# Kernel optimization log

Measured on AMD Instinct MI355X. Metric: run time of the kernel, lower is better.

## Reference

```python
import jax, jax.numpy as jnp
import numpy as np

B = 8
N_PER = 8192   # xyz points per batch
M_PER = 2048   # query points per batch
C_FEAT = 32
RADIUS = 0.2
K = 32         # sample_nums
USE_XYZ = True


def setup_inputs() -> dict:
    key = jax.random.key(0)
    k1, k2, k3 = jax.random.split(key, 3)
    xyz = jax.random.uniform(k1, (B * N_PER, 3), dtype=jnp.float32)
    new_xyz = jax.random.uniform(k2, (B * M_PER, 3), dtype=jnp.float32)
    features = jax.random.normal(k3, (B * N_PER, C_FEAT), dtype=jnp.float32)
    xyz_batch_cnt = jnp.full((B,), N_PER, dtype=jnp.int32)
    new_xyz_batch_cnt = jnp.full((B,), M_PER, dtype=jnp.int32)
    return {
        "xyz": xyz,
        "xyz_batch_cnt": xyz_batch_cnt,
        "new_xyz": new_xyz,
        "new_xyz_batch_cnt": new_xyz_batch_cnt,
        "features": features,
    }


def _ball_query(xyz_b, new_b, radius, k):
    # xyz_b: (B, N, 3), new_b: (B, M, 3)
    n = xyz_b.shape[1]
    # squared pairwise distances (B, M, N)
    d2 = jnp.sum((new_b[:, :, None, :] - xyz_b[:, None, :, :]) ** 2, axis=-1)
    mask = d2 < (radius * radius)
    # first-k in-radius indices (CUDA ball_query keeps neighbors in point order)
    scores = jnp.where(mask, jnp.arange(n, dtype=jnp.int32), jnp.int32(n))
    idx_sorted = jnp.sort(scores, axis=-1)[..., :k]          # (B, M, k)
    cnt = jnp.sum(mask, axis=-1)                              # (B, M)
    empty = cnt == 0                                          # (B, M)
    first = idx_sorted[..., :1]                               # duplicate first hit
    slot = jnp.arange(k, dtype=jnp.int32)
    idx = jnp.where(slot[None, None, :] < cnt[..., None], idx_sorted, first)
    idx = jnp.where(empty[..., None], jnp.int32(0), idx)      # empty balls -> 0
    return idx, empty


def reference(xyz, xyz_batch_cnt, new_xyz, new_xyz_batch_cnt, features):
    b = xyz_batch_cnt.shape[0]
    xyz_b = xyz.reshape(b, -1, 3)          # (B, N, 3)
    new_b = new_xyz.reshape(b, -1, 3)      # (B, M, 3)
    feat_b = features.reshape(b, xyz_b.shape[1], -1)  # (B, N, C)

    idx, empty = _ball_query(xyz_b, new_b, RADIUS, K)  # (B, M, K), (B, M)

    gather = jax.vmap(lambda pts, i: pts[i])           # per-batch gather
    grouped_xyz = gather(xyz_b, idx) - new_b[:, :, None, :]   # (B, M, K, 3)
    grouped_xyz = jnp.where(empty[..., None, None], 0.0, grouped_xyz)

    grouped_feat = gather(feat_b, idx)                        # (B, M, K, C)
    grouped_feat = jnp.where(empty[..., None, None], 0.0, grouped_feat)

    if USE_XYZ:
        new_features = jnp.concatenate([grouped_xyz, grouped_feat], axis=-1)
    else:
        new_features = grouped_feat
    # (B, M, K, 3+C) -> (B*M, 3+C, K) to match torch (Mtot, C', nsample)
    m_tot = b * new_b.shape[1]
    new_features = jnp.transpose(new_features, (0, 1, 3, 2)).reshape(
        m_tot, -1, K)
    idx_flat = idx.reshape(m_tot, K)
    return new_features, idx_flat
```

## Files before the change

kernel.cpp:

```cpp
#include <hip/hip_runtime.h>

#define BATCHES   8
#define N_PER     8192
#define M_PER     2048
#define C_FEAT    32
#define KNN       32
#define R2        0.04f
#define M_TOT     (BATCHES * M_PER)
#define FEAT_OUT  (3 + C_FEAT)
#define OUT_FEAT_SZ ((size_t)M_TOT * FEAT_OUT * KNN)

__global__ __launch_bounds__(256) void sqag_fused_kernel(
    const float* __restrict__ xyz,
    const float* __restrict__ new_xyz,
    const float* __restrict__ features,
    float* __restrict__ out)
{
    __shared__ int sidx[4][KNN];

    const int wave = threadIdx.x >> 6;
    const int lane = threadIdx.x & 63;

    const int bswz   = blockIdx.x & 7;
    const int within = blockIdx.x >> 3;
    const int q = __builtin_amdgcn_readfirstlane(
        (bswz * (M_PER / 4) + within) * 4 + wave);
    const int b    = q >> 11;
    const int base = b * N_PER;

    const float px = new_xyz[q * 3 + 0];
    const float py = new_xyz[q * 3 + 1];
    const float pz = new_xyz[q * 3 + 2];

    int cnt = 0;
    int first = 0;

    const float4* pb = (const float4*)(xyz + (size_t)base * 3) + lane * 3;
    float4 c0 = pb[0], c1 = pb[1], c2 = pb[2];

    for (int cb = 0;;) {
        const bool more = (cb + 256) < N_PER;
        float4 n0, n1, n2;
        if (more) {
            const float4* pn = pb + 192;
            n0 = pn[0]; n1 = pn[1]; n2 = pn[2];
        }

        const float X[4] = { c0.x, c0.w, c1.z, c2.y };
        const float Y[4] = { c0.y, c1.x, c1.w, c2.z };
        const float Z[4] = { c0.z, c1.y, c2.x, c2.w };

        unsigned long long m[4];
        bool in[4];
        #pragma unroll
        for (int j = 0; j < 4; ++j) {
            const float dx = px - X[j];
            const float dy = py - Y[j];
            const float dz = pz - Z[j];
            const float d2 = __fadd_rn(__fadd_rn(__fmul_rn(dx, dx),
                                                 __fmul_rn(dy, dy)),
                                       __fmul_rn(dz, dz));
            in[j] = d2 < R2;
            m[j]  = __ballot(in[j]);
        }

        if (cnt == 0) {
            int f = 0x7fffffff;
            #pragma unroll
            for (int j = 0; j < 4; ++j)
                if (m[j]) {
                    const int cand = 4 * (__ffsll((long long)m[j]) - 1) + j;
                    f = (cand < f) ? cand : f;
                }
            if (f != 0x7fffffff) first = cb + f;
        }

        int below = 0;
        #pragma unroll
        for (int j = 0; j < 4; ++j)
            below += (int)__builtin_amdgcn_mbcnt_hi(
                (unsigned)(m[j] >> 32),
                __builtin_amdgcn_mbcnt_lo((unsigned)m[j], 0u));

        int r = cnt + below;
        #pragma unroll
        for (int j = 0; j < 4; ++j) {
            if (in[j]) {
                if (r < KNN) sidx[wave][r] = cb + 4 * lane + j;
                ++r;
            }
        }
        cnt += __popcll(m[0]) + __popcll(m[1]) + __popcll(m[2]) + __popcll(m[3]);

        if (cnt >= KNN || !more) break;
        pb += 192;
        cb += 256;
        c0 = n0; c1 = n1; c2 = n2;
    }

    const int pad = (cnt == 0) ? 0 : first;
    if (lane >= cnt && lane < KNN) sidx[wave][lane] = pad;
    const float zf = (cnt == 0) ? 0.0f : 1.0f;

    const int k    = lane & 31;
    const int half = lane >> 5;

    const int li = sidx[wave][k];
    const int gi = base + li;

    const float4* f = (const float4*)(features + (size_t)gi * C_FEAT + half * 16);
    const float4 v0 = f[0];
    const float4 v1 = f[1];
    const float4 v2 = f[2];
    const float4 v3 = f[3];

    const float gx = xyz[(size_t)gi * 3 + 0] - px;
    const float gy = xyz[(size_t)gi * 3 + 1] - py;
    const float gz = xyz[(size_t)gi * 3 + 2] - pz;

    float* o = out + (size_t)q * (FEAT_OUT * KNN);
    if (half == 0) {
        __builtin_nontemporal_store(zf * gx, &o[0 * KNN + k]);
        __builtin_nontemporal_store(zf * gy, &o[1 * KNN + k]);
        __builtin_nontemporal_store(zf * gz, &o[2 * KNN + k]);
        __builtin_nontemporal_store((float)li,
                                    &out[OUT_FEAT_SZ + (size_t)q * KNN + k]);
    }

    const int jb = 3 + half * 16;
    __builtin_nontemporal_store(zf * v0.x, &o[(jb +  0) * KNN + k]);
    __builtin_nontemporal_store(zf * v0.y, &o[(jb +  1) * KNN + k]);
    __builtin_nontemporal_store(zf * v0.z, &o[(jb +  2) * KNN + k]);
    __builtin_nontemporal_store(zf * v0.w, &o[(jb +  3) * KNN + k]);
    __builtin_nontemporal_store(zf * v1.x, &o[(jb +  4) * KNN + k]);
    __builtin_nontemporal_store(zf * v1.y, &o[(jb +  5) * KNN + k]);
    __builtin_nontemporal_store(zf * v1.z, &o[(jb +  6) * KNN + k]);
    __builtin_nontemporal_store(zf * v1.w, &o[(jb +  7) * KNN + k]);
    __builtin_nontemporal_store(zf * v2.x, &o[(jb +  8) * KNN + k]);
    __builtin_nontemporal_store(zf * v2.y, &o[(jb +  9) * KNN + k]);
    __builtin_nontemporal_store(zf * v2.z, &o[(jb + 10) * KNN + k]);
    __builtin_nontemporal_store(zf * v2.w, &o[(jb + 11) * KNN + k]);
    __builtin_nontemporal_store(zf * v3.x, &o[(jb + 12) * KNN + k]);
    __builtin_nontemporal_store(zf * v3.y, &o[(jb + 13) * KNN + k]);
    __builtin_nontemporal_store(zf * v3.z, &o[(jb + 14) * KNN + k]);
    __builtin_nontemporal_store(zf * v3.w, &o[(jb + 15) * KNN + k]);
}

extern "C" void kernel_launch(void* const* d_in, const int* in_sizes, int n_in,
                              void* d_out, int out_size, void* d_ws, size_t ws_size,
                              hipStream_t stream) {
    const float* xyz      = (const float*)d_in[0];
    const float* new_xyz  = (const float*)d_in[2];
    const float* features = (const float*)d_in[4];
    float* out = (float*)d_out;

    sqag_fused_kernel<<<M_TOT / 4, 256, 0, stream>>>(xyz, new_xyz, features, out);
}
```

Before: 117.3 us.

## Process two queries per wave with atomic ticket load balancing for the second

Halves the grid so each wave handles two queries from the same batch. The first query is assigned statically; the second comes from a per-batch atomic ticket counter kept in the workspace, so waves that finish early pick up remaining queries. The per-chunk ranking and index writes are also skipped when a chunk has no in-radius hits. This adds an atomic and a block-wide barrier per query and relies on the ticket counter wrapping modulo 1024 across launches.

Measured after the change: 123.5 us. 1.05x slower.

```diff
diff --git a/kernel.cpp b/kernel.cpp
--- a/kernel.cpp
+++ b/kernel.cpp
@@ -9,11 +9,14 @@
 #define M_TOT     (BATCHES * M_PER)
 #define FEAT_OUT  (3 + C_FEAT)
 #define OUT_FEAT_SZ ((size_t)M_TOT * FEAT_OUT * KNN)
+#define WS_NEEDED  (BATCHES * 32 * sizeof(int))
 
+template <bool TICKET>
 __global__ __launch_bounds__(256) void sqag_fused_kernel(
     const float* __restrict__ xyz,
     const float* __restrict__ new_xyz,
     const float* __restrict__ features,
+    int* __restrict__ tickets,
     float* __restrict__ out)
 {
     __shared__ int sidx[4][KNN];
@@ -21,129 +24,150 @@
     const int wave = threadIdx.x >> 6;
     const int lane = threadIdx.x & 63;
 
-    const int bswz   = blockIdx.x & 7;
-    const int within = blockIdx.x >> 3;
-    const int q = __builtin_amdgcn_readfirstlane(
-        (bswz * (M_PER / 4) + within) * 4 + wave);
-    const int b    = q >> 11;
-    const int base = b * N_PER;
+    const int b      = blockIdx.x & 7;
+    const int widx   = ((blockIdx.x >> 3) << 2) + wave;
+    const int base   = b * N_PER;
+    const float4* const pb0 = (const float4*)(xyz + (size_t)base * 3) + lane * 3;
 
-    const float px = new_xyz[q * 3 + 0];
-    const float py = new_xyz[q * 3 + 1];
-    const float pz = new_xyz[q * 3 + 2];
+    int q = b * M_PER + widx;
+    int qnext = 0;
 
-    int cnt = 0;
-    int first = 0;
+    #pragma unroll 2
+    for (int qq = 0; qq < 2; ++qq) {
+        const float px = new_xyz[q * 3 + 0];
+        const float py = new_xyz[q * 3 + 1];
+        const float pz = new_xyz[q * 3 + 2];
 
-    const float4* pb = (const float4*)(xyz + (size_t)base * 3) + lane * 3;
-    float4 c0 = pb[0], c1 = pb[1], c2 = pb[2];
+        int cnt = 0;
+        int first = 0;
 
-    for (int cb = 0;;) {
-        const bool more = (cb + 256) < N_PER;
-        float4 n0, n1, n2;
-        if (more) {
-            const float4* pn = pb + 192;
-            n0 = pn[0]; n1 = pn[1]; n2 = pn[2];
+        const float4* pb = pb0;
+        float4 c0 = pb[0], c1 = pb[1], c2 = pb[2];
+
+        for (int cb = 0;;) {
+            const bool more = (cb + 256) < N_PER;
+            float4 n0, n1, n2;
+            if (more) {
+                const float4* pn = pb + 192;
+                n0 = pn[0]; n1 = pn[1]; n2 = pn[2];
+            }
+
+            const float X[4] = { c0.x, c0.w, c1.z, c2.y };
+            const float Y[4] = { c0.y, c1.x, c1.w, c2.z };
+            const float Z[4] = { c0.z, c1.y, c2.x, c2.w };
+
+            unsigned long long m[4];
+            bool in[4];
+            #pragma unroll
+            for (int j = 0; j < 4; ++j) {
+                const float dx = px - X[j];
+                const float dy = py - Y[j];
+                const float dz = pz - Z[j];
+                const float d2 = __fadd_rn(__fadd_rn(__fmul_rn(dx, dx),
+                                                     __fmul_rn(dy, dy)),
+                                           __fmul_rn(dz, dz));
+                in[j] = d2 < R2;
+                m[j]  = __ballot(in[j]);
+            }
+
+            if (m[0] | m[1] | m[2] | m[3]) {
+                if (cnt == 0) {
+                    int f = 0x7fffffff;
+                    #pragma unroll
+                    for (int j = 0; j < 4; ++j)
+                        if (m[j]) {
+                            const int cand = 4 * (__ffsll((long long)m[j]) - 1) + j;
+                            f = (cand < f) ? cand : f;
+                        }
+                    first = cb + f;
+                }
+
+                int below = 0;
+                #pragma unroll
+                for (int j = 0; j < 4; ++j)
+                    below += (int)__builtin_amdgcn_mbcnt_hi(
+                        (unsigned)(m[j] >> 32),
+                        __builtin_amdgcn_mbcnt_lo((unsigned)m[j], 0u));
+
+                int r = cnt + below;
+                #pragma unroll
+                for (int j = 0; j < 4; ++j) {
+                    if (in[j]) {
+                        if (r < KNN) sidx[wave][r] = cb + 4 * lane + j;
+                        ++r;
+                    }
+                }
+                cnt += __popcll(m[0]) + __popcll(m[1]) +
+                       __popcll(m[2]) + __popcll(m[3]);
+            }
+
+            if (cnt >= KNN || !more) break;
+            pb += 192;
+            cb += 256;
+            c0 = n0; c1 = n1; c2 = n2;
         }
 
-        const float X[4] = { c0.x, c0.w, c1.z, c2.y };
-        const float Y[4] = { c0.y, c1.x, c1.w, c2.z };
-        const float Z[4] = { c0.z, c1.y, c2.x, c2.w };
-
-        unsigned long long m[4];
-        bool in[4];
-        #pragma unroll
-        for (int j = 0; j < 4; ++j) {
-            const float dx = px - X[j];
-            const float dy = py - Y[j];
-            const float dz = pz - Z[j];
-            const float d2 = __fadd_rn(__fadd_rn(__fmul_rn(dx, dx),
-                                                 __fmul_rn(dy, dy)),
-                                       __fmul_rn(dz, dz));
-            in[j] = d2 < R2;
-            m[j]  = __ballot(in[j]);
+        if (qq == 0) {
+            int t = 0;
+            if (TICKET) {
+                if (lane == 0) t = atomicAdd(&tickets[b * 32], 1);
+                t = __builtin_amdgcn_readfirstlane(t);
+                qnext = b * M_PER + 1024 + (t & 1023);
+            } else {
+                qnext = b * M_PER + 1024 + widx;
+            }
         }
 
-        if (cnt == 0) {
-            int f = 0x7fffffff;
-            #pragma unroll
-            for (int j = 0; j < 4; ++j)
-                if (m[j]) {
-                    const int cand = 4 * (__ffsll((long long)m[j]) - 1) + j;
-                    f = (cand < f) ? cand : f;
-                }
-            if (f != 0x7fffffff) first = cb + f;
+        const int pad = (cnt == 0) ? 0 : first;
+        if (lane >= cnt && lane < KNN) sidx[wave][lane] = pad;
+        const float zf = (cnt == 0) ? 0.0f : 1.0f;
+
+        const int k    = lane & 31;
+        const int half = lane >> 5;
+
+        const int li = sidx[wave][k];
+        const int gi = base + li;
+
+        const float4* f = (const float4*)(features + (size_t)gi * C_FEAT + half * 16);
+        const float4 v0 = f[0];
+        const float4 v1 = f[1];
+        const float4 v2 = f[2];
+        const float4 v3 = f[3];
+
+        const float gx = xyz[(size_t)gi * 3 + 0] - px;
+        const float gy = xyz[(size_t)gi * 3 + 1] - py;
+        const float gz = xyz[(size_t)gi * 3 + 2] - pz;
+
+        float* o = out + (size_t)q * (FEAT_OUT * KNN);
+        if (half == 0) {
+            __builtin_nontemporal_store(zf * gx, &o[0 * KNN + k]);
+            __builtin_nontemporal_store(zf * gy, &o[1 * KNN + k]);
+            __builtin_nontemporal_store(zf * gz, &o[2 * KNN + k]);
+            __builtin_nontemporal_store((float)li,
+                                        &out[OUT_FEAT_SZ + (size_t)q * KNN + k]);
         }
 
-        int below = 0;
-        #pragma unroll
-        for (int j = 0; j < 4; ++j)
-            below += (int)__builtin_amdgcn_mbcnt_hi(
-                (unsigned)(m[j] >> 32),
-                __builtin_amdgcn_mbcnt_lo((unsigned)m[j], 0u));
+        const int jb = 3 + half * 16;
+        __builtin_nontemporal_store(zf * v0.x, &o[(jb +  0) * KNN + k]);
+        __builtin_nontemporal_store(zf * v0.y, &o[(jb +  1) * KNN + k]);
+        __builtin_nontemporal_store(zf * v0.z, &o[(jb +  2) * KNN + k]);
+        __builtin_nontemporal_store(zf * v0.w, &o[(jb +  3) * KNN + k]);
+        __builtin_nontemporal_store(zf * v1.x, &o[(jb +  4) * KNN + k]);
+        __builtin_nontemporal_store(zf * v1.y, &o[(jb +  5) * KNN + k]);
+        __builtin_nontemporal_store(zf * v1.z, &o[(jb +  6) * KNN + k]);
+        __builtin_nontemporal_store(zf * v1.w, &o[(jb +  7) * KNN + k]);
+        __builtin_nontemporal_store(zf * v2.x, &o[(jb +  8) * KNN + k]);
+        __builtin_nontemporal_store(zf * v2.y, &o[(jb +  9) * KNN + k]);
+        __builtin_nontemporal_store(zf * v2.z, &o[(jb + 10) * KNN + k]);
+        __builtin_nontemporal_store(zf * v2.w, &o[(jb + 11) * KNN + k]);
+        __builtin_nontemporal_store(zf * v3.x, &o[(jb + 12) * KNN + k]);
+        __builtin_nontemporal_store(zf * v3.y, &o[(jb + 13) * KNN + k]);
+        __builtin_nontemporal_store(zf * v3.z, &o[(jb + 14) * KNN + k]);
+        __builtin_nontemporal_store(zf * v3.w, &o[(jb + 15) * KNN + k]);
 
-        int r = cnt + below;
-        #pragma unroll
-        for (int j = 0; j < 4; ++j) {
-            if (in[j]) {
-                if (r < KNN) sidx[wave][r] = cb + 4 * lane + j;
-                ++r;
-            }
-        }
-        cnt += __popcll(m[0]) + __popcll(m[1]) + __popcll(m[2]) + __popcll(m[3]);
-
-        if (cnt >= KNN || !more) break;
-        pb += 192;
-        cb += 256;
-        c0 = n0; c1 = n1; c2 = n2;
+        q = qnext;
+        __syncthreads();
     }
-
-    const int pad = (cnt == 0) ? 0 : first;
-    if (lane >= cnt && lane < KNN) sidx[wave][lane] = pad;
-    const float zf = (cnt == 0) ? 0.0f : 1.0f;
-
-    const int k    = lane & 31;
-    const int half = lane >> 5;
-
-    const int li = sidx[wave][k];
-    const int gi = base + li;
-
-    const float4* f = (const float4*)(features + (size_t)gi * C_FEAT + half * 16);
-    const float4 v0 = f[0];
-    const float4 v1 = f[1];
-    const float4 v2 = f[2];
-    const float4 v3 = f[3];
-
-    const float gx = xyz[(size_t)gi * 3 + 0] - px;
-    const float gy = xyz[(size_t)gi * 3 + 1] - py;
-    const float gz = xyz[(size_t)gi * 3 + 2] - pz;
-
-    float* o = out + (size_t)q * (FEAT_OUT * KNN);
-    if (half == 0) {
-        __builtin_nontemporal_store(zf * gx, &o[0 * KNN + k]);
-        __builtin_nontemporal_store(zf * gy, &o[1 * KNN + k]);
-        __builtin_nontemporal_store(zf * gz, &o[2 * KNN + k]);
-        __builtin_nontemporal_store((float)li,
-                                    &out[OUT_FEAT_SZ + (size_t)q * KNN + k]);
-    }
-
-    const int jb = 3 + half * 16;
-    __builtin_nontemporal_store(zf * v0.x, &o[(jb +  0) * KNN + k]);
-    __builtin_nontemporal_store(zf * v0.y, &o[(jb +  1) * KNN + k]);
-    __builtin_nontemporal_store(zf * v0.z, &o[(jb +  2) * KNN + k]);
-    __builtin_nontemporal_store(zf * v0.w, &o[(jb +  3) * KNN + k]);
-    __builtin_nontemporal_store(zf * v1.x, &o[(jb +  4) * KNN + k]);
-    __builtin_nontemporal_store(zf * v1.y, &o[(jb +  5) * KNN + k]);
-    __builtin_nontemporal_store(zf * v1.z, &o[(jb +  6) * KNN + k]);
-    __builtin_nontemporal_store(zf * v1.w, &o[(jb +  7) * KNN + k]);
-    __builtin_nontemporal_store(zf * v2.x, &o[(jb +  8) * KNN + k]);
-    __builtin_nontemporal_store(zf * v2.y, &o[(jb +  9) * KNN + k]);
-    __builtin_nontemporal_store(zf * v2.z, &o[(jb + 10) * KNN + k]);
-    __builtin_nontemporal_store(zf * v2.w, &o[(jb + 11) * KNN + k]);
-    __builtin_nontemporal_store(zf * v3.x, &o[(jb + 12) * KNN + k]);
-    __builtin_nontemporal_store(zf * v3.y, &o[(jb + 13) * KNN + k]);
-    __builtin_nontemporal_store(zf * v3.z, &o[(jb + 14) * KNN + k]);
-    __builtin_nontemporal_store(zf * v3.w, &o[(jb + 15) * KNN + k]);
 }
 
 extern "C" void kernel_launch(void* const* d_in, const int* in_sizes, int n_in,
@@ -154,5 +178,11 @@
     const float* features = (const float*)d_in[4];
     float* out = (float*)d_out;
 
-    sqag_fused_kernel<<<M_TOT / 4, 256, 0, stream>>>(xyz, new_xyz, features, out);
+    if (d_ws != nullptr && ws_size >= WS_NEEDED) {
+        sqag_fused_kernel<true><<<M_TOT / 8, 256, 0, stream>>>(
+            xyz, new_xyz, features, (int*)d_ws, out);
+    } else {
+        sqag_fused_kernel<false><<<M_TOT / 8, 256, 0, stream>>>(
+            xyz, new_xyz, features, nullptr, out);
+    }
 }
```
